# Optimization experiments

Measured on AMD Instinct MI355X. Metric: run time of the kernel, lower is better.

Reference implementation:

```python
import jax, jax.numpy as jnp
import numpy as np

N_QUBITS = 4
N_LAYERS = 3
BATCH = 1048576  # 2**20; batched state vector [B, 2,2,2,2] complex64 = 128 MB


def setup_inputs() -> dict:
    key = jax.random.key(0)
    k1, k2 = jax.random.split(key)
    x = jax.random.normal(k1, (BATCH, N_QUBITS), dtype=jnp.float32)
    q_weights = jax.random.normal(k2, (N_LAYERS, N_QUBITS, 3), dtype=jnp.float32) * 0.1
    return {"x": x, "q_weights": q_weights}


def _ry_mat(theta):
    # RY(t) = [[cos t/2, -sin t/2], [sin t/2, cos t/2]]; theta: [] or [B]
    c = jnp.cos(theta * 0.5).astype(jnp.complex64)
    s = jnp.sin(theta * 0.5).astype(jnp.complex64)
    return jnp.stack([jnp.stack([c, -s], -1), jnp.stack([s, c], -1)], -2)


def _rz_mat(theta):
    # RZ(t) = diag(e^{-it/2}, e^{it/2})
    e = jnp.exp(-0.5j * theta.astype(jnp.complex64))
    z = jnp.zeros_like(e)
    return jnp.stack([jnp.stack([e, z], -1), jnp.stack([z, jnp.conj(e)], -1)], -2)


def _apply_1q(state, U, wire):
    # state: [B,2,2,2,2]; U: [2,2] (shared) or [B,2,2] (per-sample)
    ax = wire + 1
    state = jnp.moveaxis(state, ax, -1)
    if U.ndim == 3:
        state = jnp.einsum('b...o,bno->b...n', state, U)
    else:
        state = jnp.einsum('b...o,no->b...n', state, U)
    return jnp.moveaxis(state, -1, ax)


def _cnot(state, c, t):
    # flip target bit on the control=1 slice
    ca, ta = c + 1, t + 1
    s0 = jnp.take(state, 0, axis=ca)
    s1 = jnp.take(state, 1, axis=ca)
    ta2 = ta if ta < ca else ta - 1
    s1 = jnp.flip(s1, axis=ta2)
    return jnp.stack([s0, s1], axis=ca)


def _circuit(x, q_weights):
    B = x.shape[0]
    xn = jnp.tanh(x) * jnp.pi  # [B, 4]
    # |0000>
    state = jnp.zeros((B,) + (2,) * N_QUBITS, dtype=jnp.complex64)
    state = state.at[:, 0, 0, 0, 0].set(1.0 + 0.0j)
    # angle encoding: RY(2x_i) then RZ(x_i), per-sample batched 2x2 gates
    for i in range(N_QUBITS):
        state = _apply_1q(state, _ry_mat(2.0 * xn[:, i]), i)
        state = _apply_1q(state, _rz_mat(xn[:, i]), i)
    # variational layers: Rot(phi,theta,omega) = RZ(omega) @ RY(theta) @ RZ(phi)
    for l in range(N_LAYERS):
        for i in range(N_QUBITS):
            phi, theta, omega = q_weights[l, i, 0], q_weights[l, i, 1], q_weights[l, i, 2]
            U = _rz_mat(omega) @ _ry_mat(theta) @ _rz_mat(phi)
            state = _apply_1q(state, U, i)
        for i in range(N_QUBITS):
            state = _cnot(state, i, (i + 1) % N_QUBITS)
    # <Z_i> = p(bit_i=0) - p(bit_i=1)
    probs = jnp.abs(state) ** 2  # [B,2,2,2,2] real
    evs = []
    for i in range(N_QUBITS):
        axes = tuple(a for a in range(1, N_QUBITS + 1) if a != i + 1)
        marg = jnp.sum(probs, axis=axes)  # [B, 2]
        evs.append(marg[:, 0] - marg[:, 1])
    return jnp.stack(evs, axis=-1).astype(jnp.float32)  # [B, 4]


def reference(x, q_weights):
    return _circuit(x, q_weights)
```

## Files before the change

### kernel.cpp

```cpp
#include <hip/hip_runtime.h>


using f16x8 = __attribute__((ext_vector_type(8))) _Float16;
using f32x4 = __attribute__((ext_vector_type(4))) float;

struct C { float r, i; };

__device__ __forceinline__ C cmul(C a, C b) {
    C o;
    o.r = fmaf(a.r, b.r, -(a.i * b.i));
    o.i = fmaf(a.r, b.i,   a.i * b.r);
    return o;
}

__device__ __forceinline__ C cmadd(float ur, float ui, float wr, float wi, C a, C b) {
    C o;
    o.r = fmaf(ur, a.r, fmaf(-ui, a.i, fmaf(wr, b.r, -(wi * b.i))));
    o.i = fmaf(ur, a.i, fmaf( ui, a.r, fmaf(wr, b.i,   wi * b.r)));
    return o;
}

template <int BP>
__device__ __forceinline__ void apply_gate(C st[16], float4 A4, float4 B4) {
#pragma unroll
    for (int i = 0; i < 8; i++) {
        const int lo = ((i >> BP) << (BP + 1)) | (i & ((1 << BP) - 1));
        const int hi = lo | (1 << BP);
        const C a = st[lo], b = st[hi];
        st[lo] = cmadd(A4.x, A4.y, A4.z, A4.w, a, b);
        st[hi] = cmadd(B4.x, B4.y, B4.z, B4.w, a, b);
    }
}

template <int CB, int TB>
__device__ __forceinline__ void cnot(C st[16]) {
#pragma unroll
    for (int i = 0; i < 16; i++) {
        if ((i & (1 << CB)) && !(i & (1 << TB))) {
            C t = st[i];
            st[i] = st[i | (1 << TB)];
            st[i | (1 << TB)] = t;
        }
    }
}

struct Enc { float r0, i0, r1, i1; };
__device__ __forceinline__ Enc encode(float xq) {
    const float ax = fabsf(xq);
    const float e  = __builtin_amdgcn_exp2f(ax * -2.8853900817779268f);
    const float r  = __builtin_amdgcn_rcpf(1.0f + e);
    const float t  = copysignf((1.0f - e) * r, xq);
    const float sh = __builtin_amdgcn_sinf(t * 0.25f);
    const float ch = __builtin_amdgcn_cosf(t * 0.25f);
    const float s  = 2.0f * sh * ch;
    const float c  = fmaf(-2.0f * sh, sh, 1.0f);
    return {c * ch, -(c * sh), s * ch, s * sh};
}

__device__ __forceinline__ void wave_lds_fence() {
    asm volatile("s_waitcnt lgkmcnt(0)" ::: "memory");
    __builtin_amdgcn_sched_barrier(0);
}

#define WS_WLO 2048
#define WS_UG0 4096
#define ROWB 80

__global__ void qcompose_kernel(const float* __restrict__ qw, float* __restrict__ ws) {
    __shared__ float4 Ug[12][2];
    const int tid = threadIdx.x;
    if (tid < 12) {
        const float phi = qw[tid * 3 + 0];
        const float th  = qw[tid * 3 + 1];
        const float om  = qw[tid * 3 + 2];
        float s, c;   __sincosf(0.5f * th, &s, &c);
        float sa, ca; __sincosf(0.5f * (phi + om), &sa, &ca);
        float sb, cb; __sincosf(0.5f * (phi - om), &sb, &cb);
        Ug[tid][0] = make_float4(c * ca, -c * sa, -s * cb, -s * sb);
        Ug[tid][1] = make_float4(s * cb, -s * sb, c * ca, c * sa);
    }
    __syncthreads();

    if (tid < 4) {
        float4* o = reinterpret_cast<float4*>(reinterpret_cast<char*>(ws) + WS_UG0);
        o[2 * tid]     = Ug[tid][0];
        o[2 * tid + 1] = Ug[tid][1];
    }

    if (tid < 16) {
        C st[16];
#pragma unroll
        for (int i = 0; i < 16; i++) { st[i].r = 0.0f; st[i].i = 0.0f; }
        st[tid].r = 1.0f;

        cnot<3, 2>(st); cnot<2, 1>(st); cnot<1, 0>(st); cnot<0, 3>(st);
        apply_gate<3>(st, Ug[4][0], Ug[4][1]);
        apply_gate<2>(st, Ug[5][0], Ug[5][1]);
        apply_gate<1>(st, Ug[6][0], Ug[6][1]);
        apply_gate<0>(st, Ug[7][0], Ug[7][1]);
        cnot<3, 2>(st); cnot<2, 1>(st); cnot<1, 0>(st); cnot<0, 3>(st);
        apply_gate<3>(st, Ug[8][0], Ug[8][1]);
        apply_gate<2>(st, Ug[9][0], Ug[9][1]);
        apply_gate<1>(st, Ug[10][0], Ug[10][1]);
        apply_gate<0>(st, Ug[11][0], Ug[11][1]);
        cnot<3, 2>(st); cnot<2, 1>(st); cnot<1, 0>(st); cnot<0, 3>(st);

        _Float16* whi = reinterpret_cast<_Float16*>(ws);
        _Float16* wlo = reinterpret_cast<_Float16*>(reinterpret_cast<char*>(ws) + WS_WLO);
        const int k0 = 2 * tid, k1 = k0 + 1;
#pragma unroll
        for (int d = 0; d < 16; d++) {
            const int j0 = 2 * d, j1 = j0 + 1;
            const float vr = st[d].r, vi = st[d].i;
            float v[4]  = {vr, vi, -vi, vr};
            int   jj[4] = {j0, j1, j0, j1};
            int   kk[4] = {k0, k0, k1, k1};
#pragma unroll
            for (int e = 0; e < 4; e++) {
                _Float16 h = (_Float16)v[e];
                _Float16 l = (_Float16)((v[e] - (float)h) * 2048.0f);
                whi[jj[e] * 32 + kk[e]] = h;
                wlo[jj[e] * 32 + kk[e]] = l;
            }
        }
    }
}

__global__ __launch_bounds__(256, 6) void qlayer_kernel(const float* __restrict__ x,
                                                        const float* __restrict__ ws,
                                                        float* __restrict__ out, int B) {
    __shared__ __align__(16) unsigned char lds[4 * 64 * ROWB];
    const int tid  = threadIdx.x;
    const int lane = tid & 63;
    const int wid  = tid >> 6;
    char* slab  = reinterpret_cast<char*>(lds) + wid * (64 * ROWB);
    char* myrow = slab + lane * ROWB;

    const char* wsb = reinterpret_cast<const char*>(ws);

    const int jrow = lane & 15;
    const int kb   = (lane >> 4) * 16;
    const f16x8 Wh0 = *reinterpret_cast<const f16x8*>(wsb + jrow * 64 + kb);
    const f16x8 Wh1 = *reinterpret_cast<const f16x8*>(wsb + (jrow + 16) * 64 + kb);
    const f16x8 Wl0 = *reinterpret_cast<const f16x8*>(wsb + WS_WLO + jrow * 64 + kb);
    const f16x8 Wl1 = *reinterpret_cast<const f16x8*>(wsb + WS_WLO + (jrow + 16) * 64 + kb);
    const float4* ug0 = reinterpret_cast<const float4*>(wsb + WS_UG0);

    const int b  = blockIdx.x * 256 + tid;
    const int bl = (b < B) ? b : (B - 1);
    const float4 xv = reinterpret_cast<const float4*>(x)[bl];
    const float xs[4] = {xv.x, xv.y, xv.z, xv.w};

    C v[4][2];
#pragma unroll
    for (int q = 0; q < 4; q++) {
        const Enc e = encode(xs[q]);
        const C a{e.r0, e.i0}, bv{e.r1, e.i1};
        const float4 A4 = ug0[2 * q], B4 = ug0[2 * q + 1];
        v[q][0] = cmadd(A4.x, A4.y, A4.z, A4.w, a, bv);
        v[q][1] = cmadd(B4.x, B4.y, B4.z, B4.w, a, bv);
    }

    C t01[4], t23[4];
#pragma unroll
    for (int i = 0; i < 4; i++) {
        t01[i] = cmul(v[0][(i >> 1) & 1], v[1][i & 1]);
        t23[i] = cmul(v[2][(i >> 1) & 1], v[3][i & 1]);
    }
    f16x8 vh[4];
#pragma unroll
    for (int i = 0; i < 16; i++) {
        const C s = cmul(t01[i >> 2], t23[i & 3]);
        vh[i >> 2][2 * (i & 3)]     = (_Float16)s.r;
        vh[i >> 2][2 * (i & 3) + 1] = (_Float16)s.i;
    }
#pragma unroll
    for (int c = 0; c < 4; c++)
        *reinterpret_cast<f16x8*>(myrow + c * 16) = vh[c];

    wave_lds_fence();

    const int g = lane >> 4;
    const float f1 = (g & 1) ? 1.0f : 0.0f;
    const float f2 = (g & 2) ? 1.0f : 0.0f;
    const f32x4 Z = {0.f, 0.f, 0.f, 0.f};
    float e0 = 0.f, e1 = 0.f, e2 = 0.f, e3 = 0.f;

#pragma unroll
    for (int n = 0; n < 4; n++) {
        const f16x8 S = *reinterpret_cast<const f16x8*>(slab + (16 * n + jrow) * ROWB + kb);
        f32x4 m0 = __builtin_amdgcn_mfma_f32_16x16x32_f16(Wh0, S, Z, 0, 0, 0);
        f32x4 l0 = __builtin_amdgcn_mfma_f32_16x16x32_f16(Wl0, S, Z, 0, 0, 0);
        f32x4 m1 = __builtin_amdgcn_mfma_f32_16x16x32_f16(Wh1, S, Z, 0, 0, 0);
        f32x4 l1 = __builtin_amdgcn_mfma_f32_16x16x32_f16(Wl1, S, Z, 0, 0, 0);

        float c0[4], c1[4];
#pragma unroll
        for (int r = 0; r < 4; r++) {
            c0[r] = fmaf(l0[r], 4.8828125e-4f, m0[r]);
            c1[r] = fmaf(l1[r], 4.8828125e-4f, m1[r]);
        }
        const float p0 = fmaf(c0[1], c0[1], c0[0] * c0[0]);
        const float p1 = fmaf(c0[3], c0[3], c0[2] * c0[2]);
        const float p2 = fmaf(c1[1], c1[1], c1[0] * c1[0]);
        const float p3 = fmaf(c1[3], c1[3], c1[2] * c1[2]);
        const float Phi  = p2 + p3;
        const float Podd = p1 + p3;
        const float Pall = Phi + p0 + p1;
        float s3 = Phi, s2 = Pall * f2, s1 = Pall * f1, s0 = Podd;
        s3 += __shfl_xor(s3, 16); s2 += __shfl_xor(s2, 16);
        s1 += __shfl_xor(s1, 16); s0 += __shfl_xor(s0, 16);
        s3 += __shfl_xor(s3, 32); s2 += __shfl_xor(s2, 32);
        s1 += __shfl_xor(s1, 32); s0 += __shfl_xor(s0, 32);
        if (g == n) { e3 = s3; e2 = s2; e1 = s1; e0 = s0; }
    }

    if (b < B) {
        float4 ev;
        ev.x = fmaf(-2.0f, e3, 1.0f);
        ev.y = fmaf(-2.0f, e2, 1.0f);
        ev.z = fmaf(-2.0f, e1, 1.0f);
        ev.w = fmaf(-2.0f, e0, 1.0f);
        reinterpret_cast<float4*>(out)[b] = ev;
    }
}

extern "C" void kernel_launch(void* const* d_in, const int* in_sizes, int n_in,
                              void* d_out, int out_size, void* d_ws, size_t ws_size,
                              hipStream_t stream) {
    const float* x  = (const float*)d_in[0];
    const float* qw = (const float*)d_in[1];
    float* out = (float*)d_out;
    float* ws  = (float*)d_ws;
    const int B = in_sizes[0] / 4;
    const int blocks = (B + 255) / 256;
    qcompose_kernel<<<1, 64, 0, stream>>>(qw, ws);
    qlayer_kernel<<<blocks, 256, 0, stream>>>(x, ws, out, B);
}
```

Baseline: 82.89 us.

## Fuse gate composition into main kernel, build unitary per block in LDS

Removes the separate single-block compose kernel and its workspace round trip. Each block now computes the 12 rotation gates and the fixed 16x16 circuit unitary (split into hi/lo fp16 halves) directly into shared memory, then runs the MFMA evaluation. This saves one kernel launch and the dependency stall between kernels. In exchange every block redoes the small composition work, adds a block-wide barrier and uses extra LDS, which could reduce occupancy.

```diff
diff --git a/kernel.cpp b/kernel.cpp
--- a/kernel.cpp
+++ b/kernel.cpp
@@ -62,13 +62,20 @@
     __builtin_amdgcn_sched_barrier(0);
 }
 
-#define WS_WLO 2048
-#define WS_UG0 4096
 #define ROWB 80
 
-__global__ void qcompose_kernel(const float* __restrict__ qw, float* __restrict__ ws) {
+__global__ __launch_bounds__(256, 6) void qlayer_kernel(const float* __restrict__ x,
+                                                        const float* __restrict__ qw,
+                                                        float* __restrict__ out, int B) {
     __shared__ float4 Ug[12][2];
-    const int tid = threadIdx.x;
+    __shared__ __align__(16) unsigned char Wh_lds[2048];
+    __shared__ __align__(16) unsigned char Wl_lds[2048];
+    __shared__ __align__(16) unsigned char slab_all[4 * 64 * ROWB];
+
+    const int tid  = threadIdx.x;
+    const int lane = tid & 63;
+    const int wid  = tid >> 6;
+
     if (tid < 12) {
         const float phi = qw[tid * 3 + 0];
         const float th  = qw[tid * 3 + 1];
@@ -79,15 +86,8 @@
         Ug[tid][0] = make_float4(c * ca, -c * sa, -s * cb, -s * sb);
         Ug[tid][1] = make_float4(s * cb, -s * sb, c * ca, c * sa);
     }
-    __syncthreads();
-
-    if (tid < 4) {
-        float4* o = reinterpret_cast<float4*>(reinterpret_cast<char*>(ws) + WS_UG0);
-        o[2 * tid]     = Ug[tid][0];
-        o[2 * tid + 1] = Ug[tid][1];
-    }
-
     if (tid < 16) {
+        wave_lds_fence();
         C st[16];
 #pragma unroll
         for (int i = 0; i < 16; i++) { st[i].r = 0.0f; st[i].i = 0.0f; }
@@ -105,46 +105,35 @@
         apply_gate<0>(st, Ug[11][0], Ug[11][1]);
         cnot<3, 2>(st); cnot<2, 1>(st); cnot<1, 0>(st); cnot<0, 3>(st);
 
-        _Float16* whi = reinterpret_cast<_Float16*>(ws);
-        _Float16* wlo = reinterpret_cast<_Float16*>(reinterpret_cast<char*>(ws) + WS_WLO);
-        const int k0 = 2 * tid, k1 = k0 + 1;
+        unsigned* whiW = reinterpret_cast<unsigned*>(Wh_lds);
+        unsigned* wloW = reinterpret_cast<unsigned*>(Wl_lds);
 #pragma unroll
         for (int d = 0; d < 16; d++) {
-            const int j0 = 2 * d, j1 = j0 + 1;
             const float vr = st[d].r, vi = st[d].i;
-            float v[4]  = {vr, vi, -vi, vr};
-            int   jj[4] = {j0, j1, j0, j1};
-            int   kk[4] = {k0, k0, k1, k1};
-#pragma unroll
-            for (int e = 0; e < 4; e++) {
-                _Float16 h = (_Float16)v[e];
-                _Float16 l = (_Float16)((v[e] - (float)h) * 2048.0f);
-                whi[jj[e] * 32 + kk[e]] = h;
-                wlo[jj[e] * 32 + kk[e]] = l;
-            }
+            const _Float16 hr  = (_Float16)vr, hi_ = (_Float16)vi;
+            const _Float16 lr  = (_Float16)((vr - (float)hr)  * 2048.0f);
+            const _Float16 li  = (_Float16)((vi - (float)hi_) * 2048.0f);
+            const unsigned uhr = (unsigned)__builtin_bit_cast(unsigned short, hr);
+            const unsigned uhi = (unsigned)__builtin_bit_cast(unsigned short, hi_);
+            const unsigned ulr = (unsigned)__builtin_bit_cast(unsigned short, lr);
+            const unsigned uli = (unsigned)__builtin_bit_cast(unsigned short, li);
+            whiW[(2 * d) * 16 + tid]     = uhr | ((uhi ^ 0x8000u) << 16);
+            whiW[(2 * d + 1) * 16 + tid] = uhi | (uhr << 16);
+            wloW[(2 * d) * 16 + tid]     = ulr | ((uli ^ 0x8000u) << 16);
+            wloW[(2 * d + 1) * 16 + tid] = uli | (ulr << 16);
         }
     }
-}
-
-__global__ __launch_bounds__(256, 6) void qlayer_kernel(const float* __restrict__ x,
-                                                        const float* __restrict__ ws,
-                                                        float* __restrict__ out, int B) {
-    __shared__ __align__(16) unsigned char lds[4 * 64 * ROWB];
-    const int tid  = threadIdx.x;
-    const int lane = tid & 63;
-    const int wid  = tid >> 6;
-    char* slab  = reinterpret_cast<char*>(lds) + wid * (64 * ROWB);
-    char* myrow = slab + lane * ROWB;
-
-    const char* wsb = reinterpret_cast<const char*>(ws);
+    __syncthreads();
 
     const int jrow = lane & 15;
     const int kb   = (lane >> 4) * 16;
-    const f16x8 Wh0 = *reinterpret_cast<const f16x8*>(wsb + jrow * 64 + kb);
-    const f16x8 Wh1 = *reinterpret_cast<const f16x8*>(wsb + (jrow + 16) * 64 + kb);
-    const f16x8 Wl0 = *reinterpret_cast<const f16x8*>(wsb + WS_WLO + jrow * 64 + kb);
-    const f16x8 Wl1 = *reinterpret_cast<const f16x8*>(wsb + WS_WLO + (jrow + 16) * 64 + kb);
-    const float4* ug0 = reinterpret_cast<const float4*>(wsb + WS_UG0);
+    const f16x8 Wh0 = *reinterpret_cast<const f16x8*>(Wh_lds + jrow * 64 + kb);
+    const f16x8 Wh1 = *reinterpret_cast<const f16x8*>(Wh_lds + (jrow + 16) * 64 + kb);
+    const f16x8 Wl0 = *reinterpret_cast<const f16x8*>(Wl_lds + jrow * 64 + kb);
+    const f16x8 Wl1 = *reinterpret_cast<const f16x8*>(Wl_lds + (jrow + 16) * 64 + kb);
+
+    char* slab  = reinterpret_cast<char*>(slab_all) + wid * (64 * ROWB);
+    char* myrow = slab + lane * ROWB;
 
     const int b  = blockIdx.x * 256 + tid;
     const int bl = (b < B) ? b : (B - 1);
@@ -156,7 +145,7 @@
     for (int q = 0; q < 4; q++) {
         const Enc e = encode(xs[q]);
         const C a{e.r0, e.i0}, bv{e.r1, e.i1};
-        const float4 A4 = ug0[2 * q], B4 = ug0[2 * q + 1];
+        const float4 A4 = Ug[q][0], B4 = Ug[q][1];
         v[q][0] = cmadd(A4.x, A4.y, A4.z, A4.w, a, bv);
         v[q][1] = cmadd(B4.x, B4.y, B4.z, B4.w, a, bv);
     }
@@ -231,9 +220,7 @@
     const float* x  = (const float*)d_in[0];
     const float* qw = (const float*)d_in[1];
     float* out = (float*)d_out;
-    float* ws  = (float*)d_ws;
     const int B = in_sizes[0] / 4;
     const int blocks = (B + 255) / 256;
-    qcompose_kernel<<<1, 64, 0, stream>>>(qw, ws);
-    qlayer_kernel<<<blocks, 256, 0, stream>>>(x, ws, out, B);
-}
+    qlayer_kernel<<<blocks, 256, 0, stream>>>(x, qw, out, B);
+}
```

New measurement: 126.9 us. +53.1%, slower.
